# Kernel optimization log

Measured on AMD Instinct MI355X. Metric: run time of the kernel, lower is better.

The kernel has to match this reference:

```python
import jax, jax.numpy as jnp
import numpy as np

MARGIN = 0.3
N_GALLERY = 32768
N_BATCH = 1024
D_EMB = 512
N_CLASSES = 1000


def setup_inputs() -> dict:
    key = jax.random.key(0)
    k1, k2, k3, k4 = jax.random.split(key, 4)
    inputs = jax.random.normal(k1, (N_BATCH, D_EMB), dtype=jnp.float32)
    features = jax.random.normal(k2, (N_GALLERY, D_EMB), dtype=jnp.float32)
    feat_labels = jax.random.randint(k3, (N_GALLERY,), 0, N_CLASSES, dtype=jnp.int64 if jax.config.read('jax_enable_x64') else jnp.int32)
    idx = jax.random.randint(k4, (N_BATCH,), 0, N_GALLERY, dtype=feat_labels.dtype)
    # invariant from the original code: idx[i] is in the positive set for targets[i]
    targets = feat_labels[idx]
    return {"inputs": inputs, "features": features, "targets": targets,
            "idx": idx, "feat_labels": feat_labels}


def reference(inputs, features, targets, idx, feat_labels):
    # sim_mat: [n, N] similarity against the gallery bank
    sim = jnp.einsum('nd,Nd->nN', inputs, features)
    n = targets.shape[0]
    # positives: same label in gallery, excluding the sample's own gallery slot
    pos_mask = targets[:, None] == feat_labels[None, :]          # [n, N]
    pos_mask = pos_mask.at[jnp.arange(n), idx].set(False)
    # negatives: every gallery entry with a different label
    neg_mask = targets[:, None] != feat_labels[None, :]          # [n, N]
    pos = jnp.min(jnp.where(pos_mask, sim, jnp.inf), axis=1)     # hardest positive (lowest sim)
    neg = jnp.max(jnp.where(neg_mask, sim, -jnp.inf), axis=1)    # hardest negative (highest sim)
    loss = jnp.maximum(neg - pos + MARGIN, 0.0)
    return jnp.mean(loss)
```

## Files before the change

### kernel.cpp

```cpp
#include <hip/hip_runtime.h>
#include <stdint.h>

#define MARGIN 0.3f
#define M 1024
#define NG 32768
#define K 512
#define BM 128
#define BN 128
#define BK 64
#define NT (NG / BN)
#define NPART (NT * 2)

typedef __attribute__((ext_vector_type(8))) __bf16 bf16x8;
typedef __attribute__((ext_vector_type(4))) float f32x4;
typedef unsigned short ushort_t;
typedef unsigned int uint_t;

static __device__ __forceinline__ ushort_t f2bf(float f) {
    uint_t u = __float_as_uint(f);
    u += 0x7FFFu + ((u >> 16) & 1u);
    return (ushort_t)(u >> 16);
}

__global__ __launch_bounds__(256) void cvt_kernel(const float* __restrict__ src,
                                                  ushort_t* __restrict__ dst, int n8) {
    int i = blockIdx.x * 256 + threadIdx.x;
    if (i >= n8) return;
    const float4* s4 = (const float4*)src;
    float4 a = s4[2 * i];
    float4 b = s4[2 * i + 1];
    uint4 o;
    o.x = (uint_t)f2bf(a.x) | ((uint_t)f2bf(a.y) << 16);
    o.y = (uint_t)f2bf(a.z) | ((uint_t)f2bf(a.w) << 16);
    o.z = (uint_t)f2bf(b.x) | ((uint_t)f2bf(b.y) << 16);
    o.w = (uint_t)f2bf(b.z) | ((uint_t)f2bf(b.w) << 16);
    ((uint4*)dst)[i] = o;
}

static __device__ __forceinline__ void gload_lds16(const void* gptr, void* lptr) {
    __builtin_amdgcn_global_load_lds(
        (const __attribute__((address_space(1))) uint32_t*)(gptr),
        (__attribute__((address_space(3))) uint32_t*)(uintptr_t)(lptr),
        16, 0, 0);
}

__global__ __launch_bounds__(256) void gemm_kernel(
    const ushort_t* __restrict__ A,
    const ushort_t* __restrict__ B,
    const int* __restrict__ targets,
    const int* __restrict__ idxv,
    const int* __restrict__ labels,
    float* __restrict__ pos_part,
    float* __restrict__ neg_part) {

    __shared__ __align__(16) ushort_t sA[BM * BK];
    __shared__ __align__(16) ushort_t sB[BN * BK];
    __shared__ int t_s[BM];
    __shared__ int i_s[BM];
    __shared__ int l_s[BN];

    const int tid = threadIdx.x;
    const int lane = tid & 63;
    const int w = tid >> 6;
    const int wm = w >> 1;
    const int wn = w & 1;
    const int bid = blockIdx.x;
    const int mtile = bid & 7;
    const int ntile = bid >> 3;

    if (tid < BM) {
        t_s[tid] = targets[mtile * BM + tid];
        i_s[tid] = idxv[mtile * BM + tid];
    } else {
        l_s[tid - BM] = labels[ntile * BN + (tid - BM)];
    }

    f32x4 zero = {0.f, 0.f, 0.f, 0.f};
    f32x4 acc[4][4];
#pragma unroll
    for (int a = 0; a < 4; ++a)
#pragma unroll
        for (int b = 0; b < 4; ++b) acc[a][b] = zero;

    const int lrow8 = lane >> 3;
    const int lcol = (lane & 7) * 8;

#pragma unroll 1
    for (int kt = 0; kt < K / BK; ++kt) {
        const int kk = kt * BK;
#pragma unroll
        for (int i = 0; i < 4; ++i) {
            const int c = i * 4 + w;
            const int row = c * 8 + lrow8;
            gload_lds16(&A[(size_t)(mtile * BM + row) * K + kk + lcol], &sA[c * 512]);
            gload_lds16(&B[(size_t)(ntile * BN + row) * K + kk + lcol], &sB[c * 512]);
        }
        __syncthreads();
#pragma unroll
        for (int k2 = 0; k2 < 2; ++k2) {
            bf16x8 av[4], bv[4];
#pragma unroll
            for (int mf = 0; mf < 4; ++mf)
                av[mf] = *(const bf16x8*)&sA[(wm * 64 + mf * 16 + (lane & 15)) * BK + k2 * 32 + (lane >> 4) * 8];
#pragma unroll
            for (int nf = 0; nf < 4; ++nf)
                bv[nf] = *(const bf16x8*)&sB[(wn * 64 + nf * 16 + (lane & 15)) * BK + k2 * 32 + (lane >> 4) * 8];
#pragma unroll
            for (int mf = 0; mf < 4; ++mf)
#pragma unroll
                for (int nf = 0; nf < 4; ++nf)
                    acc[mf][nf] = __builtin_amdgcn_mfma_f32_16x16x32_bf16(av[mf], bv[nf], acc[mf][nf], 0, 0, 0);
        }
        __syncthreads();
    }

    const int l15 = lane & 15;
    const int lhi = lane >> 4;
    int labv[4], jv[4];
#pragma unroll
    for (int nf = 0; nf < 4; ++nf) {
        const int cl = wn * 64 + nf * 16 + l15;
        labv[nf] = l_s[cl];
        jv[nf] = ntile * BN + cl;
    }
#pragma unroll
    for (int mf = 0; mf < 4; ++mf) {
#pragma unroll
        for (int r = 0; r < 4; ++r) {
            const int row_l = wm * 64 + mf * 16 + lhi * 4 + r;
            const int tgt = t_s[row_l];
            const int exc = i_s[row_l];
            float pmin = INFINITY, nmax = -INFINITY;
#pragma unroll
            for (int nf = 0; nf < 4; ++nf) {
                const float v = acc[mf][nf][r];
                const bool same = (labv[nf] == tgt);
                pmin = fminf(pmin, (same && (jv[nf] != exc)) ? v : INFINITY);
                nmax = fmaxf(nmax, same ? -INFINITY : v);
            }
#pragma unroll
            for (int s = 1; s < 16; s <<= 1) {
                pmin = fminf(pmin, __shfl_xor(pmin, s, 64));
                nmax = fmaxf(nmax, __shfl_xor(nmax, s, 64));
            }
            if (l15 == 0) {
                const int row_g = mtile * BM + row_l;
                pos_part[(size_t)row_g * NPART + ntile * 2 + wn] = pmin;
                neg_part[(size_t)row_g * NPART + ntile * 2 + wn] = nmax;
            }
        }
    }
}

__global__ __launch_bounds__(256) void rowred_kernel(const float* __restrict__ pos_part,
                                                     const float* __restrict__ neg_part,
                                                     float* __restrict__ loss) {
    const int row = blockIdx.x;
    const int t = threadIdx.x;
    const float* pp = pos_part + (size_t)row * NPART;
    const float* nn = neg_part + (size_t)row * NPART;
    float p = fminf(pp[t], pp[t + 256]);
    float nx = fmaxf(nn[t], nn[t + 256]);
#pragma unroll
    for (int s = 1; s < 64; s <<= 1) {
        p = fminf(p, __shfl_xor(p, s, 64));
        nx = fmaxf(nx, __shfl_xor(nx, s, 64));
    }
    __shared__ float sp[4], sn[4];
    if ((t & 63) == 0) { sp[t >> 6] = p; sn[t >> 6] = nx; }
    __syncthreads();
    if (t == 0) {
        p = fminf(fminf(sp[0], sp[1]), fminf(sp[2], sp[3]));
        nx = fmaxf(fmaxf(sn[0], sn[1]), fmaxf(sn[2], sn[3]));
        const float l = nx - p + MARGIN;
        loss[row] = l > 0.f ? l : 0.f;
    }
}

__global__ __launch_bounds__(256) void final_kernel(const float* __restrict__ loss,
                                                    float* __restrict__ out) {
    const int t = threadIdx.x;
    float s = loss[t] + loss[t + 256] + loss[t + 512] + loss[t + 768];
#pragma unroll
    for (int sh = 1; sh < 64; sh <<= 1) s += __shfl_xor(s, sh, 64);
    __shared__ float sb[4];
    if ((t & 63) == 0) sb[t >> 6] = s;
    __syncthreads();
    if (t == 0) out[0] = (sb[0] + sb[1] + sb[2] + sb[3]) * (1.0f / 1024.0f);
}

extern "C" void kernel_launch(void* const* d_in, const int* in_sizes, int n_in,
                              void* d_out, int out_size, void* d_ws, size_t ws_size,
                              hipStream_t stream) {
    const float* inputs = (const float*)d_in[0];
    const float* features = (const float*)d_in[1];
    const int* targets = (const int*)d_in[2];
    const int* idxv = (const int*)d_in[3];
    const int* labels = (const int*)d_in[4];

    char* ws = (char*)d_ws;
    ushort_t* A = (ushort_t*)ws;
    ushort_t* B = (ushort_t*)(ws + (1u << 20));
    float* pos_part = (float*)(ws + (1u << 20) + (32u << 20));
    float* neg_part = pos_part + (size_t)M * NPART;
    float* loss = neg_part + (size_t)M * NPART;

    cvt_kernel<<<(NG * K / 8) / 256, 256, 0, stream>>>(features, B, NG * K / 8);
    cvt_kernel<<<(M * K / 8) / 256, 256, 0, stream>>>(inputs, A, M * K / 8);

    gemm_kernel<<<(M / BM) * (NG / BN), 256, 0, stream>>>(A, B, targets, idxv, labels,
                                                          pos_part, neg_part);

    rowred_kernel<<<M, 256, 0, stream>>>(pos_part, neg_part, loss);
    final_kernel<<<1, 256, 0, stream>>>(loss, (float*)d_out);
}
```

Baseline: 185.4 us.

## Double-buffer GEMM LDS tiles, merge conversion kernels, fold final mean into atomics

Double-buffers the shared-memory A/B tiles so the asynchronous global-to-LDS loads for the next K step are issued while MFMAs run on the current one, removing one barrier per iteration. Swaps the block-index mapping so consecutive blocks share the same A tile and walk along N. Merges the two fp32-to-bf16 conversion launches into one grid-stride kernel, and replaces the final mean kernel with per-row atomicAdd after a memset. This cuts launches but makes the float sum order nondeterministic and doubles LDS use, which may lower occupancy.

```diff
diff --git a/kernel.cpp b/kernel.cpp
--- a/kernel.cpp
+++ b/kernel.cpp
@@ -8,6 +8,7 @@
 #define BM 128
 #define BN 128
 #define BK 64
+#define KT (K / BK)
 #define NT (NG / BN)
 #define NPART (NT * 2)
 
@@ -22,19 +23,27 @@
     return (ushort_t)(u >> 16);
 }
 
-__global__ __launch_bounds__(256) void cvt_kernel(const float* __restrict__ src,
-                                                  ushort_t* __restrict__ dst, int n8) {
-    int i = blockIdx.x * 256 + threadIdx.x;
-    if (i >= n8) return;
-    const float4* s4 = (const float4*)src;
-    float4 a = s4[2 * i];
-    float4 b = s4[2 * i + 1];
-    uint4 o;
-    o.x = (uint_t)f2bf(a.x) | ((uint_t)f2bf(a.y) << 16);
-    o.y = (uint_t)f2bf(a.z) | ((uint_t)f2bf(a.w) << 16);
-    o.z = (uint_t)f2bf(b.x) | ((uint_t)f2bf(b.y) << 16);
-    o.w = (uint_t)f2bf(b.z) | ((uint_t)f2bf(b.w) << 16);
-    ((uint4*)dst)[i] = o;
+__global__ __launch_bounds__(256) void cvt_kernel(const float* __restrict__ fa,
+                                                  ushort_t* __restrict__ da, int n8a,
+                                                  const float* __restrict__ fb,
+                                                  ushort_t* __restrict__ db, int n8b) {
+    const int stride = gridDim.x * 256;
+    const int ntot = n8a + n8b;
+    for (int i = blockIdx.x * 256 + threadIdx.x; i < ntot; i += stride) {
+        const float4* s4;
+        uint4* d4;
+        int j;
+        if (i < n8a) { s4 = (const float4*)fa; d4 = (uint4*)da; j = i; }
+        else         { s4 = (const float4*)fb; d4 = (uint4*)db; j = i - n8a; }
+        float4 a = s4[2 * j];
+        float4 b = s4[2 * j + 1];
+        uint4 o;
+        o.x = (uint_t)f2bf(a.x) | ((uint_t)f2bf(a.y) << 16);
+        o.y = (uint_t)f2bf(a.z) | ((uint_t)f2bf(a.w) << 16);
+        o.z = (uint_t)f2bf(b.x) | ((uint_t)f2bf(b.y) << 16);
+        o.w = (uint_t)f2bf(b.z) | ((uint_t)f2bf(b.w) << 16);
+        d4[j] = o;
+    }
 }
 
 static __device__ __forceinline__ void gload_lds16(const void* gptr, void* lptr) {
@@ -53,8 +62,8 @@
     float* __restrict__ pos_part,
     float* __restrict__ neg_part) {
 
-    __shared__ __align__(16) ushort_t sA[BM * BK];
-    __shared__ __align__(16) ushort_t sB[BN * BK];
+    __shared__ __align__(16) ushort_t sA[2][BM * BK];
+    __shared__ __align__(16) ushort_t sB[2][BN * BK];
     __shared__ int t_s[BM];
     __shared__ int i_s[BM];
     __shared__ int l_s[BN];
@@ -65,8 +74,8 @@
     const int wm = w >> 1;
     const int wn = w & 1;
     const int bid = blockIdx.x;
-    const int mtile = bid & 7;
-    const int ntile = bid >> 3;
+    const int ntile = bid & 255;
+    const int mtile = bid >> 8;
 
     if (tid < BM) {
         t_s[tid] = targets[mtile * BM + tid];
@@ -84,27 +93,36 @@
 
     const int lrow8 = lane >> 3;
     const int lcol = (lane & 7) * 8;
-
-#pragma unroll 1
-    for (int kt = 0; kt < K / BK; ++kt) {
+    const ushort_t* Abase = A + (size_t)mtile * BM * K;
+    const ushort_t* Bbase = B + (size_t)ntile * BN * K;
+
+    auto stage = [&](int buf, int kt) {
         const int kk = kt * BK;
 #pragma unroll
         for (int i = 0; i < 4; ++i) {
             const int c = i * 4 + w;
             const int row = c * 8 + lrow8;
-            gload_lds16(&A[(size_t)(mtile * BM + row) * K + kk + lcol], &sA[c * 512]);
-            gload_lds16(&B[(size_t)(ntile * BN + row) * K + kk + lcol], &sB[c * 512]);
+            gload_lds16(&Abase[(size_t)row * K + kk + lcol], &sA[buf][c * 512]);
+            gload_lds16(&Bbase[(size_t)row * K + kk + lcol], &sB[buf][c * 512]);
         }
-        __syncthreads();
+    };
+
+    stage(0, 0);
+    __syncthreads();
+
+    int cur = 0;
+#pragma unroll 1
+    for (int kt = 0; kt < KT; ++kt) {
+        if (kt + 1 < KT) stage(cur ^ 1, kt + 1);
 #pragma unroll
         for (int k2 = 0; k2 < 2; ++k2) {
             bf16x8 av[4], bv[4];
 #pragma unroll
             for (int mf = 0; mf < 4; ++mf)
-                av[mf] = *(const bf16x8*)&sA[(wm * 64 + mf * 16 + (lane & 15)) * BK + k2 * 32 + (lane >> 4) * 8];
+                av[mf] = *(const bf16x8*)&sA[cur][(wm * 64 + mf * 16 + (lane & 15)) * BK + k2 * 32 + (lane >> 4) * 8];
 #pragma unroll
             for (int nf = 0; nf < 4; ++nf)
-                bv[nf] = *(const bf16x8*)&sB[(wn * 64 + nf * 16 + (lane & 15)) * BK + k2 * 32 + (lane >> 4) * 8];
+                bv[nf] = *(const bf16x8*)&sB[cur][(wn * 64 + nf * 16 + (lane & 15)) * BK + k2 * 32 + (lane >> 4) * 8];
 #pragma unroll
             for (int mf = 0; mf < 4; ++mf)
 #pragma unroll
@@ -112,6 +130,7 @@
                     acc[mf][nf] = __builtin_amdgcn_mfma_f32_16x16x32_bf16(av[mf], bv[nf], acc[mf][nf], 0, 0, 0);
         }
         __syncthreads();
+        cur ^= 1;
     }
 
     const int l15 = lane & 15;
@@ -154,7 +173,7 @@
 
 __global__ __launch_bounds__(256) void rowred_kernel(const float* __restrict__ pos_part,
                                                      const float* __restrict__ neg_part,
-                                                     float* __restrict__ loss) {
+                                                     float* __restrict__ out) {
     const int row = blockIdx.x;
     const int t = threadIdx.x;
     const float* pp = pos_part + (size_t)row * NPART;
@@ -173,20 +192,8 @@
         p = fminf(fminf(sp[0], sp[1]), fminf(sp[2], sp[3]));
         nx = fmaxf(fmaxf(sn[0], sn[1]), fmaxf(sn[2], sn[3]));
         const float l = nx - p + MARGIN;
-        loss[row] = l > 0.f ? l : 0.f;
-    }
-}
-
-__global__ __launch_bounds__(256) void final_kernel(const float* __restrict__ loss,
-                                                    float* __restrict__ out) {
-    const int t = threadIdx.x;
-    float s = loss[t] + loss[t + 256] + loss[t + 512] + loss[t + 768];
-#pragma unroll
-    for (int sh = 1; sh < 64; sh <<= 1) s += __shfl_xor(s, sh, 64);
-    __shared__ float sb[4];
-    if ((t & 63) == 0) sb[t >> 6] = s;
-    __syncthreads();
-    if (t == 0) out[0] = (sb[0] + sb[1] + sb[2] + sb[3]) * (1.0f / 1024.0f);
+        atomicAdd(out, (l > 0.f ? l : 0.f) * (1.0f / (float)M));
+    }
 }
 
 extern "C" void kernel_launch(void* const* d_in, const int* in_sizes, int n_in,
@@ -203,14 +210,13 @@
     ushort_t* B = (ushort_t*)(ws + (1u << 20));
     float* pos_part = (float*)(ws + (1u << 20) + (32u << 20));
     float* neg_part = pos_part + (size_t)M * NPART;
-    float* loss = neg_part + (size_t)M * NPART;
-
-    cvt_kernel<<<(NG * K / 8) / 256, 256, 0, stream>>>(features, B, NG * K / 8);
-    cvt_kernel<<<(M * K / 8) / 256, 256, 0, stream>>>(inputs, A, M * K / 8);
+
+    hipMemsetAsync(d_out, 0, sizeof(float), stream);
+
+    cvt_kernel<<<2048, 256, 0, stream>>>(inputs, A, M * K / 8, features, B, NG * K / 8);
 
     gemm_kernel<<<(M / BM) * (NG / BN), 256, 0, stream>>>(A, B, targets, idxv, labels,
                                                           pos_part, neg_part);
 
-    rowred_kernel<<<M, 256, 0, stream>>>(pos_part, neg_part, loss);
-    final_kernel<<<1, 256, 0, stream>>>(loss, (float*)d_out);
-}
+    rowred_kernel<<<M, 256, 0, stream>>>(pos_part, neg_part, (float*)d_out);
+}
```

Result: slower. 195.4 us (+5.4%).
